# Performance work log

Hardware: AMD Instinct MI355X
Metric: run time of the kernel (lower is better)

Reference implementation:

```python
import jax, jax.numpy as jnp
import numpy as np

DT_RANK, D_STATE, D_INNER, D_MODEL, MAMBA_SQE = 32, 16, 128, 64, 12
CHUNKS = (4, 4, 4)


def conv2d(x, w, stride=1, pad=1, groups=1, b=None):
    out = jax.lax.conv_general_dilated(x, w, (stride, stride), [(pad, pad), (pad, pad)],
                                       dimension_numbers=('NCHW', 'OIHW', 'NCHW'),
                                       feature_group_count=groups)
    return out if b is None else out + b[None, :, None, None]


def batchnorm(x, g, b, eps=1e-5):
    # training-mode BN: biased batch stats over (N, H, W)
    m = x.mean((0, 2, 3), keepdims=True)
    v = ((x - m) ** 2).mean((0, 2, 3), keepdims=True)
    return (x - m) * jax.lax.rsqrt(v + eps) * g[None, :, None, None] + b[None, :, None, None]


def layernorm(x, g, b, eps=1e-5):
    m = x.mean(-1, keepdims=True)
    v = ((x - m) ** 2).mean(-1, keepdims=True)
    return (x - m) * jax.lax.rsqrt(v + eps) * g + b


def mamba_chunk(x, state, in_w, conv_w, conv_b, xproj_w, dt_w, dt_b, A_log, D, out_w):
    # x: (B, L, d_model); state: (B, d_inner, d_state). Selective scan seeded with carried ssm_state.
    xz = jnp.einsum('bld,ed->ble', x, in_w)            # (B, L, 2*d_inner)
    xi, z = jnp.split(xz, 2, axis=-1)
    xi = jax.nn.silu(xi * conv_w + conv_b)             # depthwise conv1d with d_conv=1
    xdb = jnp.einsum('bld,ed->ble', xi, xproj_w)       # (B, L, dt_rank + 2*d_state)
    dt = xdb[..., :DT_RANK]
    Bm = xdb[..., DT_RANK:DT_RANK + D_STATE]
    Cm = xdb[..., DT_RANK + D_STATE:]
    dt = jax.nn.softplus(jnp.einsum('blr,dr->bld', dt, dt_w) + dt_b)  # (B, L, d_inner)
    A = -jnp.exp(A_log)                                # (d_inner, d_state)

    def step(st, inp):
        dt_t, x_t, B_t, C_t = inp
        dA = jnp.exp(dt_t[:, :, None] * A)             # (B, d_inner, d_state)
        st = st * dA + (dt_t * x_t)[:, :, None] * B_t[:, None, :]
        y = jnp.einsum('bdn,bn->bd', st, C_t) + D * x_t
        return st, y

    state, ys = jax.lax.scan(step, state, (dt.transpose(1, 0, 2), xi.transpose(1, 0, 2),
                                           Bm.transpose(1, 0, 2), Cm.transpose(1, 0, 2)))
    y = ys.transpose(1, 0, 2) * jax.nn.silu(z)
    return jnp.einsum('bld,ed->ble', y, out_w), state


def _forward(features, high_feature, fid0, fid1, bn_in_g, bn_in_b, down_w, down_bn_g, down_bn_b,
             emb_w, emb_b, ln1_g, ln1_b, m_in_w, m_conv_w, m_conv_b, m_xproj_w, m_dt_w, m_dt_b,
             m_A_log, m_D, m_out_w, ln2_g, ln2_b, dec_w, dec_b, up0_w, up0_bn_g, up0_bn_b,
             up1_w, up1_bn_g, up1_bn_b, fus0_w, fus0_b, fus0_bn_g, fus0_bn_b,
             fus1_w, fus1_b, fus1_bn_g, fus1_bn_b, outf_w, outf_b, expanded_ratio, out_sqe_num):
    f = features + jnp.tile(high_feature, (1, expanded_ratio, 1, 1))
    f = jnp.concatenate([high_feature, f], axis=1)          # index != 'd3_0'
    f = batchnorm(f, bn_in_g, bn_in_b)
    # downsample_size = 1
    f = jax.nn.silu(batchnorm(conv2d(f, down_w, stride=2, groups=MAMBA_SQE), down_bn_g, down_bn_b))
    f = conv2d(f, emb_w, groups=MAMBA_SQE, b=emb_b)          # (b, 12*64, h, w)
    b_, c_, h_, w_ = f.shape
    tok = f.transpose(0, 2, 3, 1).reshape(b_ * h_ * w_, MAMBA_SQE, D_MODEL)  # (b h w) s d
    mfi = tok[:, -out_sqe_num:]
    tok = layernorm(tok, ln1_g, ln1_b)
    state = jnp.zeros((b_ * h_ * w_, D_INNER, D_STATE), dtype=tok.dtype)
    outs, off, record = [], 0, False
    for i, L in enumerate(CHUNKS):
        if off == MAMBA_SQE - out_sqe_num:
            record = True
        o, state = mamba_chunk(tok[:, off:off + L], state, m_in_w[i], m_conv_w[i], m_conv_b[i],
                               m_xproj_w[i], m_dt_w[i], m_dt_b[i], m_A_log[i], m_D[i], m_out_w[i])
        if record:
            outs.append(o)
        off += L
    y = layernorm(mfi + jnp.concatenate(outs, axis=1), ln2_g, ln2_b)  # (B, out_sqe_num, d)
    y = y.reshape(b_, h_, w_, out_sqe_num * D_MODEL).transpose(0, 3, 1, 2)
    y = conv2d(y, dec_w, groups=4, b=dec_b)                  # (b, 128, h, w)
    finals = []
    for mid, fid, (uw, ug, ub), (fw, fb, fg, fbb) in zip(
            (y[:, :64], y[:, 64:]), (fid0, fid1),
            ((up0_w, up0_bn_g, up0_bn_b), (up1_w, up1_bn_g, up1_bn_b)),
            ((fus0_w, fus0_b, fus0_bn_g, fus0_bn_b), (fus1_w, fus1_b, fus1_bn_g, fus1_bn_b))):
        m = jnp.repeat(jnp.repeat(mid, 2, axis=2), 2, axis=3)  # nearest x2 (2**downsample_size)
        m = jax.nn.silu(batchnorm(conv2d(m, uw, pad=0), ug, ub))
        m = jnp.concatenate([m, fid], axis=1)
        m = jax.nn.silu(batchnorm(conv2d(m, fw, b=fb), fg, fbb))
        finals.append(m)
    out = conv2d(jnp.concatenate(finals, axis=1), outf_w, pad=0, b=outf_b)
    return jax.nn.silu(out)


def setup_inputs():
    ks = iter(jax.random.split(jax.random.key(0), 64))
    r = lambda shape, s=0.05: s * jax.random.normal(next(ks), shape, dtype=jnp.float32)
    inp = {}
    inp['features'] = jax.random.normal(next(ks), (10, 192, 64, 64), dtype=jnp.float32)
    inp['high_feature'] = jax.random.normal(next(ks), (10, 48, 64, 64), dtype=jnp.float32)
    inp['fid0'] = jax.random.normal(next(ks), (10, 64, 64, 64), dtype=jnp.float32)
    inp['fid1'] = jax.random.normal(next(ks), (10, 64, 64, 64), dtype=jnp.float32)
    inp['bn_in_g'] = 1.0 + r((240,), 0.01); inp['bn_in_b'] = r((240,), 0.01)
    inp['down_w'] = r((384, 20, 3, 3))
    inp['down_bn_g'] = 1.0 + r((384,), 0.01); inp['down_bn_b'] = r((384,), 0.01)
    inp['emb_w'] = r((768, 32, 3, 3)); inp['emb_b'] = r((768,))
    inp['ln1_g'] = 1.0 + r((64,), 0.01); inp['ln1_b'] = r((64,), 0.01)
    inp['m_in_w'] = r((3, 256, 64))
    inp['m_conv_w'] = 1.0 + r((3, 128), 0.01); inp['m_conv_b'] = r((3, 128), 0.01)
    inp['m_xproj_w'] = r((3, 64, 128)); inp['m_dt_w'] = r((3, 128, 32))
    inp['m_dt_b'] = jnp.full((3, 128), -2.0) + r((3, 128), 0.01)
    inp['m_A_log'] = jnp.tile(jnp.log(jnp.arange(1.0, 17.0, dtype=jnp.float32)), (3, 128, 1))
    inp['m_D'] = 1.0 + r((3, 128), 0.01); inp['m_out_w'] = r((3, 64, 128))
    inp['ln2_g'] = 1.0 + r((64,), 0.01); inp['ln2_b'] = r((64,), 0.01)
    inp['dec_w'] = r((128, 64, 3, 3)); inp['dec_b'] = r((128,))
    inp['up0_w'] = r((64, 64, 1, 1)); inp['up0_bn_g'] = 1.0 + r((64,), 0.01); inp['up0_bn_b'] = r((64,), 0.01)
    inp['up1_w'] = r((64, 64, 1, 1)); inp['up1_bn_g'] = 1.0 + r((64,), 0.01); inp['up1_bn_b'] = r((64,), 0.01)
    inp['fus0_w'] = r((64, 128, 3, 3)); inp['fus0_b'] = r((64,))
    inp['fus0_bn_g'] = 1.0 + r((64,), 0.01); inp['fus0_bn_b'] = r((64,), 0.01)
    inp['fus1_w'] = r((64, 128, 3, 3)); inp['fus1_b'] = r((64,))
    inp['fus1_bn_g'] = 1.0 + r((64,), 0.01); inp['fus1_bn_b'] = r((64,), 0.01)
    inp['outf_w'] = r((64, 128, 1, 1)); inp['outf_b'] = r((64,))
    inp['expanded_ratio'] = 4
    inp['out_sqe_num'] = 4
    return inp


def reference(features, high_feature, fid0, fid1, bn_in_g, bn_in_b, down_w, down_bn_g, down_bn_b,
              emb_w, emb_b, ln1_g, ln1_b, m_in_w, m_conv_w, m_conv_b, m_xproj_w, m_dt_w, m_dt_b,
              m_A_log, m_D, m_out_w, ln2_g, ln2_b, dec_w, dec_b, up0_w, up0_bn_g, up0_bn_b,
              up1_w, up1_bn_g, up1_bn_b, fus0_w, fus0_b, fus0_bn_g, fus0_bn_b,
              fus1_w, fus1_b, fus1_bn_g, fus1_bn_b, outf_w, outf_b, expanded_ratio, out_sqe_num):
    return _forward(features, high_feature, fid0, fid1, bn_in_g, bn_in_b, down_w, down_bn_g, down_bn_b,
                    emb_w, emb_b, ln1_g, ln1_b, m_in_w, m_conv_w, m_conv_b, m_xproj_w, m_dt_w, m_dt_b,
                    m_A_log, m_D, m_out_w, ln2_g, ln2_b, dec_w, dec_b, up0_w, up0_bn_g, up0_bn_b,
                    up1_w, up1_bn_g, up1_bn_b, fus0_w, fus0_b, fus0_bn_g, fus0_bn_b,
                    fus1_w, fus1_b, fus1_bn_g, fus1_bn_b, outf_w, outf_b, expanded_ratio, out_sqe_num)
```

## Files before the change

### kernel.cpp

```cpp
#include <hip/hip_runtime.h>
#include <math.h>

static __device__ __forceinline__ float silu_f(float x){
    return x * __builtin_amdgcn_rcpf(1.f + __expf(-x));
}
static __device__ __forceinline__ float softplus_f(float x){
    return (x > 20.f) ? x : __logf(1.f + __expf(x));
}

#define OFF_INT    8192u
#define OFF_WDTT   57344u
#define OFF_BCT    106496u
#define OFF_OUTT   118784u
#define OFF_A2     126976u
#define OFF_DECIN  5251072u
#define OFF_DOWN   9838592u
#define OFF_DECOUT 9838592u
#define OFF_UC0    11149312u
#define OFF_UC1    11804672u
#define OFF_TOK    13770752u
#define OFF_FUS0   13770752u
#define OFF_FUS1   16392192u

__global__ __launch_bounds__(256) void k_bn_in(const float* __restrict__ feat,
// ... 134 lines not shown
        float x6 = tp[34], x7 = tp[35], x8 = tp[36];
        const float* wpi = wb + i*9;
        #pragma unroll
        for (int oo = 0; oo < 8; ++oo){
            const float* wp = wpi + (size_t)oo*180;
            acc[oo] = fmaf(x0, wp[0], acc[oo]);
            acc[oo] = fmaf(x1, wp[1], acc[oo]);
            acc[oo] = fmaf(x2, wp[2], acc[oo]);
            acc[oo] = fmaf(x3, wp[3], acc[oo]);
            acc[oo] = fmaf(x4, wp[4], acc[oo]);
            acc[oo] = fmaf(x5, wp[5], acc[oo]);
            acc[oo] = fmaf(x6, wp[6], acc[oo]);
            acc[oo] = fmaf(x7, wp[7], acc[oo]);
            acc[oo] = fmaf(x8, wp[8], acc[oo]);
        }
    }

    int oh = oh0 + sh, ow = ow0 + sw;
    float* op = out + ((size_t)b*384 + g*32 + og*8)*1024 + (oh << 5) + ow;
    #pragma unroll
    for (int oo = 0; oo < 8; ++oo) op[(size_t)oo*1024] = acc[oo];
}

__global__ __launch_bounds__(256) void k_emb(const float* __restrict__ down_act,
                                             const float* __restrict__ w,
                                             const float* __restrict__ bias,
                                             float* __restrict__ tok){
    __shared__ float ts[3200];
    int bt = blockIdx.x;
    int b  = bt / 192;
    int rem = bt - b*192;
    int g  = rem >> 4;
    int tIdx = rem & 15;
    int oh0 = (tIdx >> 2) << 3, ow0 = (tIdx & 3) << 3;
    int tid = threadIdx.x;

    for (int j = tid; j < 3200; j += 256){
        int i = j / 100, p = j - i*100;
        int ph = p / 10, pw = p - ph*10;
        int gh = oh0 + ph - 1, gw = ow0 + pw - 1;
        float v = 0.f;
        if (gh >= 0 && gh < 32 && gw >= 0 && gw < 32)
            v = down_act[((size_t)b*384 + g*32 + i)*1024 + (gh << 5) + gw];
        ts[j] = v;
    }
    __syncthreads();

    int og = __builtin_amdgcn_readfirstlane(tid >> 6);
    int sp = tid & 63, sh = sp >> 3, sw = sp & 7;
    const float* wb = w + ((size_t)g*64 + og*16)*288;
    const float* bb = bias + g*64 + og*16;

    float acc[16];
    #pragma unroll
    for (int oo = 0; oo < 16; ++oo) acc[oo] = bb[oo];

    const float* tbase = ts + sh*10 + sw;
    #pragma unroll 2
    for (int i = 0; i < 32; ++i){
        const float* tp = tbase + i*100;
        float x0 = tp[0],  x1 = tp[1],  x2 = tp[2];
        float x3 = tp[10], x4 = tp[11], x5 = tp[12];
        float x6 = tp[20], x7 = tp[21], x8 = tp[22];
        const float* wpi = wb + i*9;
        #pragma unroll
        for (int oo = 0; oo < 16; ++oo){
// ... 42 lines not shown
        int c = j >> 14, rem = j & 16383;
        int d = rem >> 7, ch = rem & 127;
        const float* dwr = dt_w + (size_t)(c*128 + ch)*32;
        const float* xw  = xproj_w + (size_t)c*8192 + d;
        float acc = 0.f;
        #pragma unroll
        for (int r = 0; r < 32; ++r) acc = fmaf(dwr[r], xw[(size_t)r*128], acc);
        WdtT[j] = acc;
    } else if (idx < 110592){
        int j = idx - 98304;
        int c = j >> 12, rem = j & 4095;
        int d = rem >> 5, e = rem & 31;
        bcT[j] = xproj_w[((size_t)(c*64 + 32 + e))*128 + d];
    } else if (idx < 118784){
        int j = idx - 110592;
        int ch = j >> 6, e = j & 63;
        outT[j] = out_w[((size_t)(128 + e))*128 + ch];
    } else {
        int j = idx - 118784;
        A2[j] = -expf(A_log[j]);
    }
}

__global__ __launch_bounds__(128) void k_mamba8(const float* __restrict__ tok,
                                                const float* __restrict__ inT,
                                                const float* __restrict__ conv_w,
                                                const float* __restrict__ conv_b,
                                                const float* __restrict__ WdtT,
                                                const float* __restrict__ bcT,
                                                const float* __restrict__ dt_b,
                                                const float* __restrict__ A2,
                                                const float* __restrict__ Dp,
                                                const float* __restrict__ outT,
                                                const float* __restrict__ ln1_g,
                                                const float* __restrict__ ln1_b,
                                                const float* __restrict__ ln2_g,
                                                const float* __restrict__ ln2_b,
                                                float* __restrict__ dec_in){
    int token = blockIdx.x;
    int tid   = threadIdx.x;
    int lane  = tid & 63, wv = tid >> 6;
    int ch    = tid;

    __shared__ float xs[12][64];
    __shared__ float raw[4][64];
    __shared__ float xi[12][128];
    __shared__ float bcs[4][32];
    __shared__ float yz[4][128];

    const float* trow = tok + (size_t)token*768;
    for (int r = wv; r < 12; r += 2){
        float v = trow[r*64 + lane];
        if (r >= 8) raw[r-8][lane] = v;
        float m  = wsum64(v) * (1.f/64.f);
        float dv = v - m;
        float var = wsum64(dv*dv) * (1.f/64.f);
        xs[r][lane] = dv*rsqrtf(var + 1e-5f)*ln1_g[lane] + ln1_b[lane];
    }
    __syncthreads();

    for (int c = 0; c < 3; ++c){
        const float* wp = inT + (size_t)c*16384 + ch;
        float a0=0.f, a1=0.f, a2=0.f, a3=0.f;
        int s0 = c*4;
        #pragma unroll 2
        for (int d4 = 0; d4 < 16; ++d4){
            float w0 = wp[(d4*4+0)*256], w1 = wp[(d4*4+1)*256];
            float w2 = wp[(d4*4+2)*256], w3 = wp[(d4*4+3)*256];
            float4 x0 = *(const float4*)&xs[s0+0][d4*4];
            float4 x1 = *(const float4*)&xs[s0+1][d4*4];
            float4 x2 = *(const float4*)&xs[s0+2][d4*4];
            float4 x3 = *(const float4*)&xs[s0+3][d4*4];
            a0 = fmaf(x0.x,w0, fmaf(x0.y,w1, fmaf(x0.z,w2, fmaf(x0.w,w3, a0))));
            a1 = fmaf(x1.x,w0, fmaf(x1.y,w1, fmaf(x1.z,w2, fmaf(x1.w,w3, a1))));
            a2 = fmaf(x2.x,w0, fmaf(x2.y,w1, fmaf(x2.z,w2, fmaf(x2.w,w3, a2))));
            a3 = fmaf(x3.x,w0, fmaf(x3.y,w1, fmaf(x3.z,w2, fmaf(x3.w,w3, a3))));
        }
        float cw = conv_w[c*128 + ch], cb = conv_b[c*128 + ch];
        xi[s0+0][ch] = silu_f(fmaf(a0, cw, cb));
        xi[s0+1][ch] = silu_f(fmaf(a1, cw, cb));
        xi[s0+2][ch] = silu_f(fmaf(a2, cw, cb));
        xi[s0+3][ch] = silu_f(fmaf(a3, cw, cb));
    }
    float zr0=0.f, zr1=0.f, zr2=0.f, zr3=0.f;
    {
        const float* wp = inT + (size_t)2*16384 + 128 + ch;
        #pragma unroll 2
        for (int d4 = 0; d4 < 16; ++d4){
            float w0 = wp[(d4*4+0)*256], w1 = wp[(d4*4+1)*256];
            float w2 = wp[(d4*4+2)*256], w3 = wp[(d4*4+3)*256];
            float4 x0 = *(const float4*)&xs[8][d4*4];
            float4 x1 = *(const float4*)&xs[9][d4*4];
            float4 x2 = *(const float4*)&xs[10][d4*4];
            float4 x3 = *(const float4*)&xs[11][d4*4];
            zr0 = fmaf(x0.x,w0, fmaf(x0.y,w1, fmaf(x0.z,w2, fmaf(x0.w,w3, zr0))));
            zr1 = fmaf(x1.x,w0, fmaf(x1.y,w1, fmaf(x1.z,w2, fmaf(x1.w,w3, zr1))));
            zr2 = fmaf(x2.x,w0, fmaf(x2.y,w1, fmaf(x2.z,w2, fmaf(x2.w,w3, zr2))));
            zr3 = fmaf(x3.x,w0, fmaf(x3.y,w1, fmaf(x3.z,w2, fmaf(x3.w,w3, zr3))));
        }
        zr0 = silu_f(zr0); zr1 = silu_f(zr1); zr2 = silu_f(zr2); zr3 = silu_f(zr3);
    }
    __syncthreads();

    int sidx = tid >> 5, be = tid & 31;
    float st[16];
    #pragma unroll
    for (int n = 0; n < 16; ++n) st[n] = 0.f;

    for (int c = 0; c < 3; ++c){
        int s0 = c*4;
        float dts0, dts1, dts2, dts3;
        {
            const float* wp = WdtT + (size_t)c*16384 + ch;
            float a0=0.f, a1=0.f, a2=0.f, a3=0.f;
            #pragma unroll 2
            for (int d4 = 0; d4 < 32; ++d4){
                float w0 = wp[(d4*4+0)*128], w1 = wp[(d4*4+1)*128];
                float w2 = wp[(d4*4+2)*128], w3 = wp[(d4*4+3)*128];
                float4 x0 = *(const float4*)&xi[s0+0][d4*4];
                float4 x1 = *(const float4*)&xi[s0+1][d4*4];
                float4 x2 = *(const float4*)&xi[s0+2][d4*4];
                float4 x3 = *(const float4*)&xi[s0+3][d4*4];
                a0 = fmaf(x0.x,w0, fmaf(x0.y,w1, fmaf(x0.z,w2, fmaf(x0.w,w3, a0))));
                a1 = fmaf(x1.x,w0, fmaf(x1.y,w1, fmaf(x1.z,w2, fmaf(x1.w,w3, a1))));
                a2 = fmaf(x2.x,w0, fmaf(x2.y,w1, fmaf(x2.z,w2, fmaf(x2.w,w3, a2))));
                a3 = fmaf(x3.x,w0, fmaf(x3.y,w1, fmaf(x3.z,w2, fmaf(x3.w,w3, a3))));
            }
            float db = dt_b[c*128 + ch];
            dts0 = softplus_f(a0 + db);
            dts1 = softplus_f(a1 + db);
            dts2 = softplus_f(a2 + db);
            dts3 = softplus_f(a3 + db);
        }
        float bcacc = 0.f;
        {
            const float* wp = bcT + (size_t)c*4096 + be;
            #pragma unroll 2
            for (int d4 = 0; d4 < 32; ++d4){
                float w0 = wp[(d4*4+0)*32], w1 = wp[(d4*4+1)*32];
                float w2 = wp[(d4*4+2)*32], w3 = wp[(d4*4+3)*32];
                float4 x = *(const float4*)&xi[s0+sidx][d4*4];
                bcacc = fmaf(x.x,w0, fmaf(x.y,w1, fmaf(x.z,w2, fmaf(x.w,w3, bcacc))));
            }
        }
        __syncthreads();
        bcs[sidx][be] = bcacc;
        __syncthreads();

        float A_[16];
        {
            const float4* ap = (const float4*)(A2 + ((size_t)c*128 + ch)*16);
            float4 a0v = ap[0], a1v = ap[1], a2v = ap[2], a3v = ap[3];
            A_[0]=a0v.x; A_[1]=a0v.y; A_[2]=a0v.z; A_[3]=a0v.w;
            A_[4]=a1v.x; A_[5]=a1v.y; A_[6]=a1v.z; A_[7]=a1v.w;
            A_[8]=a2v.x; A_[9]=a2v.y; A_[10]=a2v.z; A_[11]=a2v.w;
            A_[12]=a3v.x; A_[13]=a3v.y; A_[14]=a3v.z; A_[15]=a3v.w;
        }
        float Dch = Dp[c*128 + ch];

        #pragma unroll
        for (int t = 0; t < 4; ++t){
            float dtc = (t==0)?dts0:((t==1)?dts1:((t==2)?dts2:dts3));
            float xiv = xi[s0+t][ch];
            float dx  = dtc * xiv;
            float4 b0 = *(const float4*)&bcs[t][0];
            float4 b1 = *(const float4*)&bcs[t][4];
            float4 b2 = *(const float4*)&bcs[t][8];
            float4 b3 = *(const float4*)&bcs[t][12];
            if (c < 2){
                st[0] = fmaf(st[0],  __expf(dtc*A_[0]),  dx*b0.x);
                st[1] = fmaf(st[1],  __expf(dtc*A_[1]),  dx*b0.y);
                st[2] = fmaf(st[2],  __expf(dtc*A_[2]),  dx*b0.z);
                st[3] = fmaf(st[3],  __expf(dtc*A_[3]),  dx*b0.w);
                st[4] = fmaf(st[4],  __expf(dtc*A_[4]),  dx*b1.x);
                st[5] = fmaf(st[5],  __expf(dtc*A_[5]),  dx*b1.y);
                st[6] = fmaf(st[6],  __expf(dtc*A_[6]),  dx*b1.z);
                st[7] = fmaf(st[7],  __expf(dtc*A_[7]),  dx*b1.w);
                st[8] = fmaf(st[8],  __expf(dtc*A_[8]),  dx*b2.x);
                st[9] = fmaf(st[9],  __expf(dtc*A_[9]),  dx*b2.y);
                st[10]= fmaf(st[10], __expf(dtc*A_[10]), dx*b2.z);
                st[11]= fmaf(st[11], __expf(dtc*A_[11]), dx*b2.w);
                st[12]= fmaf(st[12], __expf(dtc*A_[12]), dx*b3.x);
                st[13]= fmaf(st[13], __expf(dtc*A_[13]), dx*b3.y);
                st[14]= fmaf(st[14], __expf(dtc*A_[14]), dx*b3.z);
                st[15]= fmaf(st[15], __expf(dtc*A_[15]), dx*b3.w);
            } else {
                float4 c0 = *(const float4*)&bcs[t][16];
                float4 c1 = *(const float4*)&bcs[t][20];
                float4 c2 = *(const float4*)&bcs[t][24];
                float4 c3 = *(const float4*)&bcs[t][28];
                float y = 0.f;
                st[0] = fmaf(st[0],  __expf(dtc*A_[0]),  dx*b0.x); y = fmaf(st[0],  c0.x, y);
                st[1] = fmaf(st[1],  __expf(dtc*A_[1]),  dx*b0.y); y = fmaf(st[1],  c0.y, y);
                st[2] = fmaf(st[2],  __expf(dtc*A_[2]),  dx*b0.z); y = fmaf(st[2],  c0.z, y);
                st[3] = fmaf(st[3],  __expf(dtc*A_[3]),  dx*b0.w); y = fmaf(st[3],  c0.w, y);
                st[4] = fmaf(st[4],  __expf(dtc*A_[4]),  dx*b1.x); y = fmaf(st[4],  c1.x, y);
                st[5] = fmaf(st[5],  __expf(dtc*A_[5]),  dx*b1.y); y = fmaf(st[5],  c1.y, y);
                st[6] = fmaf(st[6],  __expf(dtc*A_[6]),  dx*b1.z); y = fmaf(st[6],  c1.z, y);
                st[7] = fmaf(st[7],  __expf(dtc*A_[7]),  dx*b1.w); y = fmaf(st[7],  c1.w, y);
                st[8] = fmaf(st[8],  __expf(dtc*A_[8]),  dx*b2.x); y = fmaf(st[8],  c2.x, y);
                st[9] = fmaf(st[9],  __expf(dtc*A_[9]),  dx*b2.y); y = fmaf(st[9],  c2.y, y);
                st[10]= fmaf(st[10], __expf(dtc*A_[10]), dx*b2.z); y = fmaf(st[10], c2.z, y);
                st[11]= fmaf(st[11], __expf(dtc*A_[11]), dx*b2.w); y = fmaf(st[11], c2.w, y);
                st[12]= fmaf(st[12], __expf(dtc*A_[12]), dx*b3.x); y = fmaf(st[12], c3.x, y);
                st[13]= fmaf(st[13], __expf(dtc*A_[13]), dx*b3.y); y = fmaf(st[13], c3.y, y);
                st[14]= fmaf(st[14], __expf(dtc*A_[14]), dx*b3.z); y = fmaf(st[14], c3.z, y);
                st[15]= fmaf(st[15], __expf(dtc*A_[15]), dx*b3.w); y = fmaf(st[15], c3.w, y);
                y = fmaf(Dch, xiv, y);
                float zr = (t==0)?zr0:((t==1)?zr1:((t==2)?zr2:zr3));
                yz[t][ch] = y * zr;
            }
        }
    }
    __syncthreads();

    int b = token >> 10, hw = token & 1023;
    int e = tid & 63, l2 = tid >> 6;
    #pragma unroll
    for (int p = 0; p < 2; ++p){
        int l = l2*2 + p;
        float acc = 0.f;
        const float* wp = outT + e;
        #pragma unroll 2
        for (int k4 = 0; k4 < 32; ++k4){
            float w0 = wp[(k4*4+0)*64], w1 = wp[(k4*4+1)*64];
            float w2 = wp[(k4*4+2)*64], w3 = wp[(k4*4+3)*64];
            float4 y = *(const float4*)&yz[l][k4*4];
            acc = fmaf(y.x,w0, fmaf(y.y,w1, fmaf(y.z,w2, fmaf(y.w,w3, acc))));
        }
        float v = raw[l][e] + acc;
        float m  = wsum64(v) * (1.f/64.f);
        float dv = v - m;
        float var = wsum64(dv*dv) * (1.f/64.f);
        float r = dv*rsqrtf(var + 1e-5f)*ln2_g[e] + ln2_b[e];
        dec_in[(size_t)b*262144 + (size_t)(l*64 + e)*1024 + hw] = r;
    }
}

__global__ __launch_bounds__(256) void k_dec(const float* __restrict__ dec_in,
                                             const float* __restrict__ w,
                                             const float* __restrict__ bias,
                                             float* __restrict__ out){
    __shared__ float ts[6400];
    int bt = blockIdx.x;
    int b  = bt >> 6;
    int rem = bt & 63;
    int g  = rem >> 4;
    int tIdx = rem & 15;
    int oh0 = (tIdx >> 2) << 3, ow0 = (tIdx & 3) << 3;
    int tid = threadIdx.x;

    for (int j = tid; j < 6400; j += 256){
        int i = j / 100, p = j - i*100;
        int ph = p / 10, pw = p - ph*10;
        int gh = oh0 + ph - 1, gw = ow0 + pw - 1;
        float v = 0.f;
        if (gh >= 0 && gh < 32 && gw >= 0 && gw < 32)
            v = dec_in[((size_t)b*256 + g*64 + i)*1024 + (gh << 5) + gw];
// ... 41 lines not shown

__global__ __launch_bounds__(256) void k_up(const float* __restrict__ dec_out,
                                            const float* __restrict__ w0,
                                            const float* __restrict__ w1,
                                            float* __restrict__ uc0,
                                            float* __restrict__ uc1){
    int idx = blockIdx.x*256 + threadIdx.x;
    int r = idx >= 655360;
    int j = idx - r*655360;
    int b   = j / 65536;
    int rem = j - b*65536;
    int o   = rem >> 10;
    int hw  = rem & 1023;
    __shared__ float w_s[64];
    if (threadIdx.x < 64) w_s[threadIdx.x] = (r ? w1 : w0)[o*64 + threadIdx.x];
    __syncthreads();
    const float* in = dec_out + (size_t)b*131072 + (size_t)(r*64)*1024 + hw;
    float acc = 0.f;
    #pragma unroll 8
    for (int i = 0; i < 64; ++i) acc = fmaf(in[(size_t)i*1024], w_s[i], acc);
    (r ? uc1 : uc0)[j] = acc;
}

__global__ __launch_bounds__(256) void k_fus(const float* __restrict__ uc_act,
                                             const float* __restrict__ fid,
                                             const float* __restrict__ w,
                                             const float* __restrict__ bias,
                                             float* __restrict__ out){
    __shared__ float ts[12800];
    int bt = blockIdx.x;
    int b  = bt >> 6, tIdx = bt & 63;
    int oh0 = (tIdx >> 3) << 3, ow0 = (tIdx & 7) << 3;
    int tid = threadIdx.x;

    for (int j = tid; j < 12800; j += 256){
        int i = j / 100, p = j - i*100;
        int ph = p / 10, pw = p - ph*10;
        int gh = oh0 + ph - 1, gw = ow0 + pw - 1;
        float v = 0.f;
        if (gh >= 0 && gh < 64 && gw >= 0 && gw < 64){
            if (i < 64) v = uc_act[(((size_t)b*64 + i) << 10) + ((gh >> 1) << 5) + (gw >> 1)];
            else        v = fid[(((size_t)b*64 + i - 64) << 12) + (gh << 6) + gw];
        }
        ts[j] = v;
    }
    __syncthreads();

    int og = __builtin_amdgcn_readfirstlane(tid >> 6);
    int sp = tid & 63, sh = sp >> 3, sw = sp & 7;
    const float* wb = w + (size_t)og * 18432;
    const float* bb = bias + og * 16;

    float acc[16];
    #pragma unroll
    for (int oo = 0; oo < 16; ++oo) acc[oo] = bb[oo];

    const float* tbase = ts + sh*10 + sw;
    #pragma unroll 2
    for (int i = 0; i < 128; ++i){
        const float* tp = tbase + i*100;
        float x0 = tp[0],  x1 = tp[1],  x2 = tp[2];
        float x3 = tp[10], x4 = tp[11], x5 = tp[12];
        float x6 = tp[20], x7 = tp[21], x8 = tp[22];
        const float* wpi = wb + i*9;
        #pragma unroll
// ... 95 lines not shown
    float* st_u1_sc  = ws + 1664; float* st_u1_sh  = ws + 1728;
    float* st_f0_sc  = ws + 1792; float* st_f0_sh  = ws + 1856;
    float* st_f1_sc  = ws + 1920; float* st_f1_sh  = ws + 1984;

    float* inT    = ws + OFF_INT;
    float* WdtT   = ws + OFF_WDTT;
    float* bcT    = ws + OFF_BCT;
    float* outT   = ws + OFF_OUTT;
    float* A2     = ws + OFF_A2;
    float* dec_in = ws + OFF_DECIN;
    float* down   = ws + OFF_DOWN;
    float* dec_out= ws + OFF_DECOUT;
    float* uc0    = ws + OFF_UC0;
    float* uc1    = ws + OFF_UC1;
    float* tok    = ws + OFF_TOK;
    float* fus0   = ws + OFF_FUS0;
    float* fus1   = ws + OFF_FUS1;

    k_prep<<<488, 256, 0, stream>>>(m_in_w, m_dt_w, m_xproj_w, m_out_w, m_A_log,
                                    inT, WdtT, bcT, outT, A2);
    k_bn_in<<<240, 256, 0, stream>>>(features, high, bn_in_g, bn_in_b, st_in_sc, st_in_sh);
    k_down<<<1920, 256, 0, stream>>>(features, high, down_w, st_in_sc, st_in_sh, down);
    k_bn_stats<<<384, 256, 0, stream>>>(down, down_bn_g, down_bn_b, st_dn_sc, st_dn_sh, 384, 10, 10);
    k_affine_silu<<<15360, 256, 0, stream>>>(down, st_dn_sc, st_dn_sh, 384, 10, 3932160);
    k_emb<<<1920, 256, 0, stream>>>(down, emb_w, emb_b, tok);
    k_mamba8<<<10240, 128, 0, stream>>>(tok, inT, m_conv_w, m_conv_b, WdtT, bcT,
                                        m_dt_b, A2, m_D, outT,
                                        ln1_g, ln1_b, ln2_g, ln2_b, dec_in);
    k_dec<<<640, 256, 0, stream>>>(dec_in, dec_w, dec_b, dec_out);
    k_up<<<5120, 256, 0, stream>>>(dec_out, up0_w, up1_w, uc0, uc1);
    k_bn_stats<<<64, 256, 0, stream>>>(uc0, up0_bn_g, up0_bn_b, st_u0_sc, st_u0_sh, 64, 10, 10);
    k_bn_stats<<<64, 256, 0, stream>>>(uc1, up1_bn_g, up1_bn_b, st_u1_sc, st_u1_sh, 64, 10, 10);
    k_affine_silu<<<2560, 256, 0, stream>>>(uc0, st_u0_sc, st_u0_sh, 64, 10, 655360);
    k_affine_silu<<<2560, 256, 0, stream>>>(uc1, st_u1_sc, st_u1_sh, 64, 10, 655360);
    k_fus<<<640, 256, 0, stream>>>(uc0, fid0, fus0_w, fus0_b, fus0);
    k_fus<<<640, 256, 0, stream>>>(uc1, fid1, fus1_w, fus1_b, fus1);
    k_bn_stats<<<64, 256, 0, stream>>>(fus0, fus0_bn_g, fus0_bn_b, st_f0_sc, st_f0_sh, 64, 12, 10);
    k_bn_stats<<<64, 256, 0, stream>>>(fus1, fus1_bn_g, fus1_bn_b, st_f1_sc, st_f1_sh, 64, 12, 10);
    k_affine_silu<<<10240, 256, 0, stream>>>(fus0, st_f0_sc, st_f0_sh, 64, 12, 2621440);
    k_affine_silu<<<10240, 256, 0, stream>>>(fus1, st_f1_sc, st_f1_sh, 64, 12, 2621440);
    k_final<<<10240, 256, 0, stream>>>(fus0, fus1, outf_w, outf_b, out);
}
```

Before: 1.249 ms.

## Fuse BN-affine+SiLU into emb/fus loads and halve mamba block to one wave

The standalone BN affine+SiLU passes over the down-conv output and the two upsample outputs are removed. The affine and SiLU are now applied while k_emb and k_fus load their input tiles, which saves three elementwise kernels and their full read/write traffic. The mamba kernel is also reworked from 128 threads (one channel each) to 64 threads that each handle two channels. This doubles per-thread registers and serial work, but lets every weight load feed two channels and keeps the whole block in one wave. Because the halo tiles overlap, the fused kernels recompute SiLU on some elements, and the mamba change may lower occupancy.

```diff
diff --git a/kernel.cpp b/kernel.cpp
--- a/kernel.cpp
+++ b/kernel.cpp
@@ -180,7 +180,9 @@
     for (int oo = 0; oo < 8; ++oo) op[(size_t)oo*1024] = acc[oo];
 }
 
-__global__ __launch_bounds__(256) void k_emb(const float* __restrict__ down_act,
+__global__ __launch_bounds__(256) void k_emb(const float* __restrict__ down_raw,
+                                             const float* __restrict__ sc,
+                                             const float* __restrict__ sh_,
                                              const float* __restrict__ w,
                                              const float* __restrict__ bias,
                                              float* __restrict__ tok){
@@ -198,8 +200,11 @@
         int ph = p / 10, pw = p - ph*10;
         int gh = oh0 + ph - 1, gw = ow0 + pw - 1;
         float v = 0.f;
-        if (gh >= 0 && gh < 32 && gw >= 0 && gw < 32)
-            v = down_act[((size_t)b*384 + g*32 + i)*1024 + (gh << 5) + gw];
+        if (gh >= 0 && gh < 32 && gw >= 0 && gw < 32){
+            int c = g*32 + i;
+            float raw = down_raw[((size_t)b*384 + c)*1024 + (gh << 5) + gw];
+            v = silu_f(fmaf(raw, sc[c], sh_[c]));
+        }
         ts[j] = v;
     }
     __syncthreads();
@@ -288,25 +293,24 @@
     }
 }
 
-__global__ __launch_bounds__(128) void k_mamba8(const float* __restrict__ tok,
-                                                const float* __restrict__ inT,
-                                                const float* __restrict__ conv_w,
-                                                const float* __restrict__ conv_b,
-                                                const float* __restrict__ WdtT,
-                                                const float* __restrict__ bcT,
-                                                const float* __restrict__ dt_b,
-                                                const float* __restrict__ A2,
-                                                const float* __restrict__ Dp,
-                                                const float* __restrict__ outT,
-                                                const float* __restrict__ ln1_g,
-                                                const float* __restrict__ ln1_b,
-                                                const float* __restrict__ ln2_g,
-                                                const float* __restrict__ ln2_b,
-                                                float* __restrict__ dec_in){
+__global__ __launch_bounds__(64) void k_mamba9(const float* __restrict__ tok,
+                                               const float* __restrict__ inT,
+                                               const float* __restrict__ conv_w,
+                                               const float* __restrict__ conv_b,
+                                               const float* __restrict__ WdtT,
+                                               const float* __restrict__ bcT,
+                                               const float* __restrict__ dt_b,
+                                               const float* __restrict__ A2,
+                                               const float* __restrict__ Dp,
+                                               const float* __restrict__ outT,
+                                               const float* __restrict__ ln1_g,
+                                               const float* __restrict__ ln1_b,
+                                               const float* __restrict__ ln2_g,
+                                               const float* __restrict__ ln2_b,
+                                               float* __restrict__ dec_in){
     int token = blockIdx.x;
     int tid   = threadIdx.x;
-    int lane  = tid & 63, wv = tid >> 6;
-    int ch    = tid;
+    int ch0 = tid, ch1 = tid + 64;
 
     __shared__ float xs[12][64];
     __shared__ float raw[4][64];
@@ -315,24 +319,27 @@
     __shared__ float yz[4][128];
 
     const float* trow = tok + (size_t)token*768;
-    for (int r = wv; r < 12; r += 2){
-        float v = trow[r*64 + lane];
-        if (r >= 8) raw[r-8][lane] = v;
+    for (int r = 0; r < 12; ++r){
+        float v = trow[r*64 + tid];
+        if (r >= 8) raw[r-8][tid] = v;
         float m  = wsum64(v) * (1.f/64.f);
         float dv = v - m;
         float var = wsum64(dv*dv) * (1.f/64.f);
-        xs[r][lane] = dv*rsqrtf(var + 1e-5f)*ln1_g[lane] + ln1_b[lane];
+        xs[r][tid] = dv*rsqrtf(var + 1e-5f)*ln1_g[tid] + ln1_b[tid];
     }
     __syncthreads();
 
     for (int c = 0; c < 3; ++c){
-        const float* wp = inT + (size_t)c*16384 + ch;
+        const float* wp0 = inT + (size_t)c*16384 + ch0;
         float a0=0.f, a1=0.f, a2=0.f, a3=0.f;
+        float a4=0.f, a5=0.f, a6=0.f, a7=0.f;
         int s0 = c*4;
         #pragma unroll 2
         for (int d4 = 0; d4 < 16; ++d4){
-            float w0 = wp[(d4*4+0)*256], w1 = wp[(d4*4+1)*256];
-            float w2 = wp[(d4*4+2)*256], w3 = wp[(d4*4+3)*256];
+            float w0 = wp0[(d4*4+0)*256],    w1 = wp0[(d4*4+1)*256];
+            float w2 = wp0[(d4*4+2)*256],    w3 = wp0[(d4*4+3)*256];
+            float w4 = wp0[(d4*4+0)*256+64], w5 = wp0[(d4*4+1)*256+64];
+            float w6 = wp0[(d4*4+2)*256+64], w7 = wp0[(d4*4+3)*256+64];
             float4 x0 = *(const float4*)&xs[s0+0][d4*4];
             float4 x1 = *(const float4*)&xs[s0+1][d4*4];
             float4 x2 = *(const float4*)&xs[s0+2][d4*4];
@@ -341,48 +348,68 @@
             a1 = fmaf(x1.x,w0, fmaf(x1.y,w1, fmaf(x1.z,w2, fmaf(x1.w,w3, a1))));
             a2 = fmaf(x2.x,w0, fmaf(x2.y,w1, fmaf(x2.z,w2, fmaf(x2.w,w3, a2))));
             a3 = fmaf(x3.x,w0, fmaf(x3.y,w1, fmaf(x3.z,w2, fmaf(x3.w,w3, a3))));
-        }
-        float cw = conv_w[c*128 + ch], cb = conv_b[c*128 + ch];
-        xi[s0+0][ch] = silu_f(fmaf(a0, cw, cb));
-        xi[s0+1][ch] = silu_f(fmaf(a1, cw, cb));
-        xi[s0+2][ch] = silu_f(fmaf(a2, cw, cb));
-        xi[s0+3][ch] = silu_f(fmaf(a3, cw, cb));
-    }
-    float zr0=0.f, zr1=0.f, zr2=0.f, zr3=0.f;
+            a4 = fmaf(x0.x,w4, fmaf(x0.y,w5, fmaf(x0.z,w6, fmaf(x0.w,w7, a4))));
+            a5 = fmaf(x1.x,w4, fmaf(x1.y,w5, fmaf(x1.z,w6, fmaf(x1.w,w7, a5))));
+            a6 = fmaf(x2.x,w4, fmaf(x2.y,w5, fmaf(x2.z,w6, fmaf(x2.w,w7, a6))));
+            a7 = fmaf(x3.x,w4, fmaf(x3.y,w5, fmaf(x3.z,w6, fmaf(x3.w,w7, a7))));
+        }
+        float cw0 = conv_w[c*128 + ch0], cb0 = conv_b[c*128 + ch0];
+        float cw1 = conv_w[c*128 + ch1], cb1 = conv_b[c*128 + ch1];
+        xi[s0+0][ch0] = silu_f(fmaf(a0, cw0, cb0));
+        xi[s0+1][ch0] = silu_f(fmaf(a1, cw0, cb0));
+        xi[s0+2][ch0] = silu_f(fmaf(a2, cw0, cb0));
+        xi[s0+3][ch0] = silu_f(fmaf(a3, cw0, cb0));
+        xi[s0+0][ch1] = silu_f(fmaf(a4, cw1, cb1));
+        xi[s0+1][ch1] = silu_f(fmaf(a5, cw1, cb1));
+        xi[s0+2][ch1] = silu_f(fmaf(a6, cw1, cb1));
+        xi[s0+3][ch1] = silu_f(fmaf(a7, cw1, cb1));
+    }
+    float za0=0.f, za1=0.f, za2=0.f, za3=0.f;
+    float zb0=0.f, zb1=0.f, zb2=0.f, zb3=0.f;
     {
-        const float* wp = inT + (size_t)2*16384 + 128 + ch;
+        const float* wp0 = inT + (size_t)2*16384 + 128 + ch0;
         #pragma unroll 2
         for (int d4 = 0; d4 < 16; ++d4){
-            float w0 = wp[(d4*4+0)*256], w1 = wp[(d4*4+1)*256];
-            float w2 = wp[(d4*4+2)*256], w3 = wp[(d4*4+3)*256];
+            float w0 = wp0[(d4*4+0)*256],    w1 = wp0[(d4*4+1)*256];
+            float w2 = wp0[(d4*4+2)*256],    w3 = wp0[(d4*4+3)*256];
+            float w4 = wp0[(d4*4+0)*256+64], w5 = wp0[(d4*4+1)*256+64];
+            float w6 = wp0[(d4*4+2)*256+64], w7 = wp0[(d4*4+3)*256+64];
             float4 x0 = *(const float4*)&xs[8][d4*4];
             float4 x1 = *(const float4*)&xs[9][d4*4];
             float4 x2 = *(const float4*)&xs[10][d4*4];
             float4 x3 = *(const float4*)&xs[11][d4*4];
-            zr0 = fmaf(x0.x,w0, fmaf(x0.y,w1, fmaf(x0.z,w2, fmaf(x0.w,w3, zr0))));
-            zr1 = fmaf(x1.x,w0, fmaf(x1.y,w1, fmaf(x1.z,w2, fmaf(x1.w,w3, zr1))));
-            zr2 = fmaf(x2.x,w0, fmaf(x2.y,w1, fmaf(x2.z,w2, fmaf(x2.w,w3, zr2))));
-            zr3 = fmaf(x3.x,w0, fmaf(x3.y,w1, fmaf(x3.z,w2, fmaf(x3.w,w3, zr3))));
-        }
-        zr0 = silu_f(zr0); zr1 = silu_f(zr1); zr2 = silu_f(zr2); zr3 = silu_f(zr3);
+            za0 = fmaf(x0.x,w0, fmaf(x0.y,w1, fmaf(x0.z,w2, fmaf(x0.w,w3, za0))));
+            za1 = fmaf(x1.x,w0, fmaf(x1.y,w1, fmaf(x1.z,w2, fmaf(x1.w,w3, za1))));
+            za2 = fmaf(x2.x,w0, fmaf(x2.y,w1, fmaf(x2.z,w2, fmaf(x2.w,w3, za2))));
+            za3 = fmaf(x3.x,w0, fmaf(x3.y,w1, fmaf(x3.z,w2, fmaf(x3.w,w3, za3))));
+            zb0 = fmaf(x0.x,w4, fmaf(x0.y,w5, fmaf(x0.z,w6, fmaf(x0.w,w7, zb0))));
+            zb1 = fmaf(x1.x,w4, fmaf(x1.y,w5, fmaf(x1.z,w6, fmaf(x1.w,w7, zb1))));
+            zb2 = fmaf(x2.x,w4, fmaf(x2.y,w5, fmaf(x2.z,w6, fmaf(x2.w,w7, zb2))));
+            zb3 = fmaf(x3.x,w4, fmaf(x3.y,w5, fmaf(x3.z,w6, fmaf(x3.w,w7, zb3))));
+        }
+        za0 = silu_f(za0); za1 = silu_f(za1); za2 = silu_f(za2); za3 = silu_f(za3);
+        zb0 = silu_f(zb0); zb1 = silu_f(zb1); zb2 = silu_f(zb2); zb3 = silu_f(zb3);
     }
     __syncthreads();
 
     int sidx = tid >> 5, be = tid & 31;
-    float st[16];
-    #pragma unroll
-    for (int n = 0; n < 16; ++n) st[n] = 0.f;
+    float st0[16], st1[16];
+    #pragma unroll
+    for (int n = 0; n < 16; ++n){ st0[n] = 0.f; st1[n] = 0.f; }
 
     for (int c = 0; c < 3; ++c){
         int s0 = c*4;
-        float dts0, dts1, dts2, dts3;
+        float dA0, dA1, dA2, dA3, dB0, dB1, dB2, dB3;
         {
-            const float* wp = WdtT + (size_t)c*16384 + ch;
+            const float* wp0 = WdtT + (size_t)c*16384 + ch0;
             float a0=0.f, a1=0.f, a2=0.f, a3=0.f;
+            float a4=0.f, a5=0.f, a6=0.f, a7=0.f;
             #pragma unroll 2
             for (int d4 = 0; d4 < 32; ++d4){
-                float w0 = wp[(d4*4+0)*128], w1 = wp[(d4*4+1)*128];
-                float w2 = wp[(d4*4+2)*128], w3 = wp[(d4*4+3)*128];
+                float w0 = wp0[(d4*4+0)*128],    w1 = wp0[(d4*4+1)*128];
+                float w2 = wp0[(d4*4+2)*128],    w3 = wp0[(d4*4+3)*128];
+                float w4 = wp0[(d4*4+0)*128+64], w5 = wp0[(d4*4+1)*128+64];
+                float w6 = wp0[(d4*4+2)*128+64], w7 = wp0[(d4*4+3)*128+64];
                 float4 x0 = *(const float4*)&xi[s0+0][d4*4];
                 float4 x1 = *(const float4*)&xi[s0+1][d4*4];
                 float4 x2 = *(const float4*)&xi[s0+2][d4*4];
@@ -391,102 +418,147 @@
                 a1 = fmaf(x1.x,w0, fmaf(x1.y,w1, fmaf(x1.z,w2, fmaf(x1.w,w3, a1))));
                 a2 = fmaf(x2.x,w0, fmaf(x2.y,w1, fmaf(x2.z,w2, fmaf(x2.w,w3, a2))));
                 a3 = fmaf(x3.x,w0, fmaf(x3.y,w1, fmaf(x3.z,w2, fmaf(x3.w,w3, a3))));
+                a4 = fmaf(x0.x,w4, fmaf(x0.y,w5, fmaf(x0.z,w6, fmaf(x0.w,w7, a4))));
+                a5 = fmaf(x1.x,w4, fmaf(x1.y,w5, fmaf(x1.z,w6, fmaf(x1.w,w7, a5))));
+                a6 = fmaf(x2.x,w4, fmaf(x2.y,w5, fmaf(x2.z,w6, fmaf(x2.w,w7, a6))));
+                a7 = fmaf(x3.x,w4, fmaf(x3.y,w5, fmaf(x3.z,w6, fmaf(x3.w,w7, a7))));
             }
-            float db = dt_b[c*128 + ch];
-            dts0 = softplus_f(a0 + db);
-            dts1 = softplus_f(a1 + db);
-            dts2 = softplus_f(a2 + db);
-            dts3 = softplus_f(a3 + db);
-        }
-        float bcacc = 0.f;
+            float db0 = dt_b[c*128 + ch0], db1 = dt_b[c*128 + ch1];
+            dA0 = softplus_f(a0 + db0); dA1 = softplus_f(a1 + db0);
+            dA2 = softplus_f(a2 + db0); dA3 = softplus_f(a3 + db0);
+            dB0 = softplus_f(a4 + db1); dB1 = softplus_f(a5 + db1);
+            dB2 = softplus_f(a6 + db1); dB3 = softplus_f(a7 + db1);
+        }
+        float bc0 = 0.f, bc1 = 0.f;
         {
             const float* wp = bcT + (size_t)c*4096 + be;
             #pragma unroll 2
             for (int d4 = 0; d4 < 32; ++d4){
                 float w0 = wp[(d4*4+0)*32], w1 = wp[(d4*4+1)*32];
                 float w2 = wp[(d4*4+2)*32], w3 = wp[(d4*4+3)*32];
-                float4 x = *(const float4*)&xi[s0+sidx][d4*4];
-                bcacc = fmaf(x.x,w0, fmaf(x.y,w1, fmaf(x.z,w2, fmaf(x.w,w3, bcacc))));
+                float4 xA = *(const float4*)&xi[s0+sidx][d4*4];
+                float4 xB = *(const float4*)&xi[s0+sidx+2][d4*4];
+                bc0 = fmaf(xA.x,w0, fmaf(xA.y,w1, fmaf(xA.z,w2, fmaf(xA.w,w3, bc0))));
+                bc1 = fmaf(xB.x,w0, fmaf(xB.y,w1, fmaf(xB.z,w2, fmaf(xB.w,w3, bc1))));
             }
         }
         __syncthreads();
-        bcs[sidx][be] = bcacc;
+        bcs[sidx][be]   = bc0;
+        bcs[sidx+2][be] = bc1;
         __syncthreads();
 
-        float A_[16];
+        float A0_[16], A1_[16];
         {
-            const float4* ap = (const float4*)(A2 + ((size_t)c*128 + ch)*16);
-            float4 a0v = ap[0], a1v = ap[1], a2v = ap[2], a3v = ap[3];
-            A_[0]=a0v.x; A_[1]=a0v.y; A_[2]=a0v.z; A_[3]=a0v.w;
-            A_[4]=a1v.x; A_[5]=a1v.y; A_[6]=a1v.z; A_[7]=a1v.w;
-            A_[8]=a2v.x; A_[9]=a2v.y; A_[10]=a2v.z; A_[11]=a2v.w;
-            A_[12]=a3v.x; A_[13]=a3v.y; A_[14]=a3v.z; A_[15]=a3v.w;
-        }
-        float Dch = Dp[c*128 + ch];
+            const float4* ap0 = (const float4*)(A2 + ((size_t)c*128 + ch0)*16);
+            const float4* ap1 = (const float4*)(A2 + ((size_t)c*128 + ch1)*16);
+            #pragma unroll
+            for (int q = 0; q < 4; ++q){
+                float4 v0 = ap0[q], v1 = ap1[q];
+                A0_[q*4+0]=v0.x; A0_[q*4+1]=v0.y; A0_[q*4+2]=v0.z; A0_[q*4+3]=v0.w;
+                A1_[q*4+0]=v1.x; A1_[q*4+1]=v1.y; A1_[q*4+2]=v1.z; A1_[q*4+3]=v1.w;
+            }
+        }
+        float D0 = Dp[c*128 + ch0], D1 = Dp[c*128 + ch1];
 
         #pragma unroll
         for (int t = 0; t < 4; ++t){
-            float dtc = (t==0)?dts0:((t==1)?dts1:((t==2)?dts2:dts3));
-            float xiv = xi[s0+t][ch];
-            float dx  = dtc * xiv;
+            float dt0 = (t==0)?dA0:((t==1)?dA1:((t==2)?dA2:dA3));
+            float dt1 = (t==0)?dB0:((t==1)?dB1:((t==2)?dB2:dB3));
+            float xv0 = xi[s0+t][ch0];
+            float xv1 = xi[s0+t][ch1];
+            float dx0 = dt0 * xv0;
+            float dx1 = dt1 * xv1;
             float4 b0 = *(const float4*)&bcs[t][0];
             float4 b1 = *(const float4*)&bcs[t][4];
             float4 b2 = *(const float4*)&bcs[t][8];
             float4 b3 = *(const float4*)&bcs[t][12];
             if (c < 2){
-                st[0] = fmaf(st[0],  __expf(dtc*A_[0]),  dx*b0.x);
-                st[1] = fmaf(st[1],  __expf(dtc*A_[1]),  dx*b0.y);
-                st[2] = fmaf(st[2],  __expf(dtc*A_[2]),  dx*b0.z);
-                st[3] = fmaf(st[3],  __expf(dtc*A_[3]),  dx*b0.w);
-                st[4] = fmaf(st[4],  __expf(dtc*A_[4]),  dx*b1.x);
-                st[5] = fmaf(st[5],  __expf(dtc*A_[5]),  dx*b1.y);
-                st[6] = fmaf(st[6],  __expf(dtc*A_[6]),  dx*b1.z);
-                st[7] = fmaf(st[7],  __expf(dtc*A_[7]),  dx*b1.w);
-                st[8] = fmaf(st[8],  __expf(dtc*A_[8]),  dx*b2.x);
-                st[9] = fmaf(st[9],  __expf(dtc*A_[9]),  dx*b2.y);
-                st[10]= fmaf(st[10], __expf(dtc*A_[10]), dx*b2.z);
-                st[11]= fmaf(st[11], __expf(dtc*A_[11]), dx*b2.w);
-                st[12]= fmaf(st[12], __expf(dtc*A_[12]), dx*b3.x);
-                st[13]= fmaf(st[13], __expf(dtc*A_[13]), dx*b3.y);
-                st[14]= fmaf(st[14], __expf(dtc*A_[14]), dx*b3.z);
-                st[15]= fmaf(st[15], __expf(dtc*A_[15]), dx*b3.w);
+                st0[0] = fmaf(st0[0],  __expf(dt0*A0_[0]),  dx0*b0.x);
+                st0[1] = fmaf(st0[1],  __expf(dt0*A0_[1]),  dx0*b0.y);
+                st0[2] = fmaf(st0[2],  __expf(dt0*A0_[2]),  dx0*b0.z);
+                st0[3] = fmaf(st0[3],  __expf(dt0*A0_[3]),  dx0*b0.w);
+                st0[4] = fmaf(st0[4],  __expf(dt0*A0_[4]),  dx0*b1.x);
+                st0[5] = fmaf(st0[5],  __expf(dt0*A0_[5]),  dx0*b1.y);
+                st0[6] = fmaf(st0[6],  __expf(dt0*A0_[6]),  dx0*b1.z);
+                st0[7] = fmaf(st0[7],  __expf(dt0*A0_[7]),  dx0*b1.w);
+                st0[8] = fmaf(st0[8],  __expf(dt0*A0_[8]),  dx0*b2.x);
+                st0[9] = fmaf(st0[9],  __expf(dt0*A0_[9]),  dx0*b2.y);
+                st0[10]= fmaf(st0[10], __expf(dt0*A0_[10]), dx0*b2.z);
+                st0[11]= fmaf(st0[11], __expf(dt0*A0_[11]), dx0*b2.w);
+                st0[12]= fmaf(st0[12], __expf(dt0*A0_[12]), dx0*b3.x);
+                st0[13]= fmaf(st0[13], __expf(dt0*A0_[13]), dx0*b3.y);
+                st0[14]= fmaf(st0[14], __expf(dt0*A0_[14]), dx0*b3.z);
+                st0[15]= fmaf(st0[15], __expf(dt0*A0_[15]), dx0*b3.w);
+                st1[0] = fmaf(st1[0],  __expf(dt1*A1_[0]),  dx1*b0.x);
+                st1[1] = fmaf(st1[1],  __expf(dt1*A1_[1]),  dx1*b0.y);
+                st1[2] = fmaf(st1[2],  __expf(dt1*A1_[2]),  dx1*b0.z);
+                st1[3] = fmaf(st1[3],  __expf(dt1*A1_[3]),  dx1*b0.w);
+                st1[4] = fmaf(st1[4],  __expf(dt1*A1_[4]),  dx1*b1.x);
+                st1[5] = fmaf(st1[5],  __expf(dt1*A1_[5]),  dx1*b1.y);
+                st1[6] = fmaf(st1[6],  __expf(dt1*A1_[6]),  dx1*b1.z);
+                st1[7] = fmaf(st1[7],  __expf(dt1*A1_[7]),  dx1*b1.w);
+                st1[8] = fmaf(st1[8],  __expf(dt1*A1_[8]),  dx1*b2.x);
+                st1[9] = fmaf(st1[9],  __expf(dt1*A1_[9]),  dx1*b2.y);
+                st1[10]= fmaf(st1[10], __expf(dt1*A1_[10]), dx1*b2.z);
+                st1[11]= fmaf(st1[11], __expf(dt1*A1_[11]), dx1*b2.w);
+                st1[12]= fmaf(st1[12], __expf(dt1*A1_[12]), dx1*b3.x);
+                st1[13]= fmaf(st1[13], __expf(dt1*A1_[13]), dx1*b3.y);
+                st1[14]= fmaf(st1[14], __expf(dt1*A1_[14]), dx1*b3.z);
+                st1[15]= fmaf(st1[15], __expf(dt1*A1_[15]), dx1*b3.w);
             } else {
                 float4 c0 = *(const float4*)&bcs[t][16];
                 float4 c1 = *(const float4*)&bcs[t][20];
                 float4 c2 = *(const float4*)&bcs[t][24];
                 float4 c3 = *(const float4*)&bcs[t][28];
-                float y = 0.f;
-                st[0] = fmaf(st[0],  __expf(dtc*A_[0]),  dx*b0.x); y = fmaf(st[0],  c0.x, y);
-                st[1] = fmaf(st[1],  __expf(dtc*A_[1]),  dx*b0.y); y = fmaf(st[1],  c0.y, y);
-                st[2] = fmaf(st[2],  __expf(dtc*A_[2]),  dx*b0.z); y = fmaf(st[2],  c0.z, y);
-                st[3] = fmaf(st[3],  __expf(dtc*A_[3]),  dx*b0.w); y = fmaf(st[3],  c0.w, y);
-                st[4] = fmaf(st[4],  __expf(dtc*A_[4]),  dx*b1.x); y = fmaf(st[4],  c1.x, y);
-                st[5] = fmaf(st[5],  __expf(dtc*A_[5]),  dx*b1.y); y = fmaf(st[5],  c1.y, y);
-                st[6] = fmaf(st[6],  __expf(dtc*A_[6]),  dx*b1.z); y = fmaf(st[6],  c1.z, y);
-                st[7] = fmaf(st[7],  __expf(dtc*A_[7]),  dx*b1.w); y = fmaf(st[7],  c1.w, y);
-                st[8] = fmaf(st[8],  __expf(dtc*A_[8]),  dx*b2.x); y = fmaf(st[8],  c2.x, y);
-                st[9] = fmaf(st[9],  __expf(dtc*A_[9]),  dx*b2.y); y = fmaf(st[9],  c2.y, y);
-                st[10]= fmaf(st[10], __expf(dtc*A_[10]), dx*b2.z); y = fmaf(st[10], c2.z, y);
-                st[11]= fmaf(st[11], __expf(dtc*A_[11]), dx*b2.w); y = fmaf(st[11], c2.w, y);
-                st[12]= fmaf(st[12], __expf(dtc*A_[12]), dx*b3.x); y = fmaf(st[12], c3.x, y);
-                st[13]= fmaf(st[13], __expf(dtc*A_[13]), dx*b3.y); y = fmaf(st[13], c3.y, y);
-                st[14]= fmaf(st[14], __expf(dtc*A_[14]), dx*b3.z); y = fmaf(st[14], c3.z, y);
-                st[15]= fmaf(st[15], __expf(dtc*A_[15]), dx*b3.w); y = fmaf(st[15], c3.w, y);
-                y = fmaf(Dch, xiv, y);
-                float zr = (t==0)?zr0:((t==1)?zr1:((t==2)?zr2:zr3));
-                yz[t][ch] = y * zr;
+                float y0 = 0.f, y1 = 0.f;
+                st0[0] = fmaf(st0[0],  __expf(dt0*A0_[0]),  dx0*b0.x); y0 = fmaf(st0[0],  c0.x, y0);
+                st0[1] = fmaf(st0[1],  __expf(dt0*A0_[1]),  dx0*b0.y); y0 = fmaf(st0[1],  c0.y, y0);
+                st0[2] = fmaf(st0[2],  __expf(dt0*A0_[2]),  dx0*b0.z); y0 = fmaf(st0[2],  c0.z, y0);
+                st0[3] = fmaf(st0[3],  __expf(dt0*A0_[3]),  dx0*b0.w); y0 = fmaf(st0[3],  c0.w, y0);
+                st0[4] = fmaf(st0[4],  __expf(dt0*A0_[4]),  dx0*b1.x); y0 = fmaf(st0[4],  c1.x, y0);
+                st0[5] = fmaf(st0[5],  __expf(dt0*A0_[5]),  dx0*b1.y); y0 = fmaf(st0[5],  c1.y, y0);
+                st0[6] = fmaf(st0[6],  __expf(dt0*A0_[6]),  dx0*b1.z); y0 = fmaf(st0[6],  c1.z, y0);
+                st0[7] = fmaf(st0[7],  __expf(dt0*A0_[7]),  dx0*b1.w); y0 = fmaf(st0[7],  c1.w, y0);
+                st0[8] = fmaf(st0[8],  __expf(dt0*A0_[8]),  dx0*b2.x); y0 = fmaf(st0[8],  c2.x, y0);
+                st0[9] = fmaf(st0[9],  __expf(dt0*A0_[9]),  dx0*b2.y); y0 = fmaf(st0[9],  c2.y, y0);
+                st0[10]= fmaf(st0[10], __expf(dt0*A0_[10]), dx0*b2.z); y0 = fmaf(st0[10], c2.z, y0);
+                st0[11]= fmaf(st0[11], __expf(dt0*A0_[11]), dx0*b2.w); y0 = fmaf(st0[11], c2.w, y0);
+                st0[12]= fmaf(st0[12], __expf(dt0*A0_[12]), dx0*b3.x); y0 = fmaf(st0[12], c3.x, y0);
+                st0[13]= fmaf(st0[13], __expf(dt0*A0_[13]), dx0*b3.y); y0 = fmaf(st0[13], c3.y, y0);
+                st0[14]= fmaf(st0[14], __expf(dt0*A0_[14]), dx0*b3.z); y0 = fmaf(st0[14], c3.z, y0);
+                st0[15]= fmaf(st0[15], __expf(dt0*A0_[15]), dx0*b3.w); y0 = fmaf(st0[15], c3.w, y0);
+                st1[0] = fmaf(st1[0],  __expf(dt1*A1_[0]),  dx1*b0.x); y1 = fmaf(st1[0],  c0.x, y1);
+                st1[1] = fmaf(st1[1],  __expf(dt1*A1_[1]),  dx1*b0.y); y1 = fmaf(st1[1],  c0.y, y1);
+                st1[2] = fmaf(st1[2],  __expf(dt1*A1_[2]),  dx1*b0.z); y1 = fmaf(st1[2],  c0.z, y1);
+                st1[3] = fmaf(st1[3],  __expf(dt1*A1_[3]),  dx1*b0.w); y1 = fmaf(st1[3],  c0.w, y1);
+                st1[4] = fmaf(st1[4],  __expf(dt1*A1_[4]),  dx1*b1.x); y1 = fmaf(st1[4],  c1.x, y1);
+                st1[5] = fmaf(st1[5],  __expf(dt1*A1_[5]),  dx1*b1.y); y1 = fmaf(st1[5],  c1.y, y1);
+                st1[6] = fmaf(st1[6],  __expf(dt1*A1_[6]),  dx1*b1.z); y1 = fmaf(st1[6],  c1.z, y1);
+                st1[7] = fmaf(st1[7],  __expf(dt1*A1_[7]),  dx1*b1.w); y1 = fmaf(st1[7],  c1.w, y1);
+                st1[8] = fmaf(st1[8],  __expf(dt1*A1_[8]),  dx1*b2.x); y1 = fmaf(st1[8],  c2.x, y1);
+                st1[9] = fmaf(st1[9],  __expf(dt1*A1_[9]),  dx1*b2.y); y1 = fmaf(st1[9],  c2.y, y1);
+                st1[10]= fmaf(st1[10], __expf(dt1*A1_[10]), dx1*b2.z); y1 = fmaf(st1[10], c2.z, y1);
+                st1[11]= fmaf(st1[11], __expf(dt1*A1_[11]), dx1*b2.w); y1 = fmaf(st1[11], c2.w, y1);
+                st1[12]= fmaf(st1[12], __expf(dt1*A1_[12]), dx1*b3.x); y1 = fmaf(st1[12], c3.x, y1);
+                st1[13]= fmaf(st1[13], __expf(dt1*A1_[13]), dx1*b3.y); y1 = fmaf(st1[13], c3.y, y1);
+                st1[14]= fmaf(st1[14], __expf(dt1*A1_[14]), dx1*b3.z); y1 = fmaf(st1[14], c3.z, y1);
+                st1[15]= fmaf(st1[15], __expf(dt1*A1_[15]), dx1*b3.w); y1 = fmaf(st1[15], c3.w, y1);
+                y0 = fmaf(D0, xv0, y0);
+                y1 = fmaf(D1, xv1, y1);
+                float zr0v = (t==0)?za0:((t==1)?za1:((t==2)?za2:za3));
+                float zr1v = (t==0)?zb0:((t==1)?zb1:((t==2)?zb2:zb3));
+                yz[t][ch0] = y0 * zr0v;
+                yz[t][ch1] = y1 * zr1v;
             }
         }
     }
     __syncthreads();
 
     int b = token >> 10, hw = token & 1023;
-    int e = tid & 63, l2 = tid >> 6;
-    #pragma unroll
-    for (int p = 0; p < 2; ++p){
-        int l = l2*2 + p;
+    #pragma unroll
+    for (int l = 0; l < 4; ++l){
         float acc = 0.f;
-        const float* wp = outT + e;
+        const float* wp = outT + tid;
         #pragma unroll 2
         for (int k4 = 0; k4 < 32; ++k4){
             float w0 = wp[(k4*4+0)*64], w1 = wp[(k4*4+1)*64];
@@ -494,12 +566,12 @@
             float4 y = *(const float4*)&yz[l][k4*4];
             acc = fmaf(y.x,w0, fmaf(y.y,w1, fmaf(y.z,w2, fmaf(y.w,w3, acc))));
         }
-        float v = raw[l][e] + acc;
+        float v = raw[l][tid] + acc;
         float m  = wsum64(v) * (1.f/64.f);
         float dv = v - m;
         float var = wsum64(dv*dv) * (1.f/64.f);
-        float r = dv*rsqrtf(var + 1e-5f)*ln2_g[e] + ln2_b[e];
-        dec_in[(size_t)b*262144 + (size_t)(l*64 + e)*1024 + hw] = r;
+        float r = dv*rsqrtf(var + 1e-5f)*ln2_g[tid] + ln2_b[tid];
+        dec_in[(size_t)b*262144 + (size_t)(l*64 + tid)*1024 + hw] = r;
     }
 }
 
@@ -587,7 +659,9 @@
     (r ? uc1 : uc0)[j] = acc;
 }
 
-__global__ __launch_bounds__(256) void k_fus(const float* __restrict__ uc_act,
+__global__ __launch_bounds__(256) void k_fus(const float* __restrict__ uc_raw,
+                                             const float* __restrict__ uc_sc,
+                                             const float* __restrict__ uc_sh,
                                              const float* __restrict__ fid,
                                              const float* __restrict__ w,
                                              const float* __restrict__ bias,
@@ -604,8 +678,12 @@
         int gh = oh0 + ph - 1, gw = ow0 + pw - 1;
         float v = 0.f;
         if (gh >= 0 && gh < 64 && gw >= 0 && gw < 64){
-            if (i < 64) v = uc_act[(((size_t)b*64 + i) << 10) + ((gh >> 1) << 5) + (gw >> 1)];
-            else        v = fid[(((size_t)b*64 + i - 64) << 12) + (gh << 6) + gw];
+            if (i < 64){
+                float raw = uc_raw[(((size_t)b*64 + i) << 10) + ((gh >> 1) << 5) + (gw >> 1)];
+                v = silu_f(fmaf(raw, uc_sc[i], uc_sh[i]));
+            } else {
+                v = fid[(((size_t)b*64 + i - 64) << 12) + (gh << 6) + gw];
+            }
         }
         ts[j] = v;
     }
@@ -747,19 +825,16 @@
     k_bn_in<<<240, 256, 0, stream>>>(features, high, bn_in_g, bn_in_b, st_in_sc, st_in_sh);
     k_down<<<1920, 256, 0, stream>>>(features, high, down_w, st_in_sc, st_in_sh, down);
     k_bn_stats<<<384, 256, 0, stream>>>(down, down_bn_g, down_bn_b, st_dn_sc, st_dn_sh, 384, 10, 10);
-    k_affine_silu<<<15360, 256, 0, stream>>>(down, st_dn_sc, st_dn_sh, 384, 10, 3932160);
-    k_emb<<<1920, 256, 0, stream>>>(down, emb_w, emb_b, tok);
-    k_mamba8<<<10240, 128, 0, stream>>>(tok, inT, m_conv_w, m_conv_b, WdtT, bcT,
-                                        m_dt_b, A2, m_D, outT,
-                                        ln1_g, ln1_b, ln2_g, ln2_b, dec_in);
+    k_emb<<<1920, 256, 0, stream>>>(down, st_dn_sc, st_dn_sh, emb_w, emb_b, tok);
+    k_mamba9<<<10240, 64, 0, stream>>>(tok, inT, m_conv_w, m_conv_b, WdtT, bcT,
+                                       m_dt_b, A2, m_D, outT,
+                                       ln1_g, ln1_b, ln2_g, ln2_b, dec_in);
     k_dec<<<640, 256, 0, stream>>>(dec_in, dec_w, dec_b, dec_out);
     k_up<<<5120, 256, 0, stream>>>(dec_out, up0_w, up1_w, uc0, uc1);
     k_bn_stats<<<64, 256, 0, stream>>>(uc0, up0_bn_g, up0_bn_b, st_u0_sc, st_u0_sh, 64, 10, 10);
     k_bn_stats<<<64, 256, 0, stream>>>(uc1, up1_bn_g, up1_bn_b, st_u1_sc, st_u1_sh, 64, 10, 10);
-    k_affine_silu<<<2560, 256, 0, stream>>>(uc0, st_u0_sc, st_u0_sh, 64, 10, 655360);
-    k_affine_silu<<<2560, 256, 0, stream>>>(uc1, st_u1_sc, st_u1_sh, 64, 10, 655360);
-    k_fus<<<640, 256, 0, stream>>>(uc0, fid0, fus0_w, fus0_b, fus0);
-    k_fus<<<640, 256, 0, stream>>>(uc1, fid1, fus1_w, fus1_b, fus1);
+    k_fus<<<640, 256, 0, stream>>>(uc0, st_u0_sc, st_u0_sh, fid0, fus0_w, fus0_b, fus0);
+    k_fus<<<640, 256, 0, stream>>>(uc1, st_u1_sc, st_u1_sh, fid1, fus1_w, fus1_b, fus1);
     k_bn_stats<<<64, 256, 0, stream>>>(fus0, fus0_bn_g, fus0_bn_b, st_f0_sc, st_f0_sh, 64, 12, 10);
     k_bn_stats<<<64, 256, 0, stream>>>(fus1, fus1_bn_g, fus1_bn_b, st_f1_sc, st_f1_sh, 64, 12, 10);
     k_affine_silu<<<10240, 256, 0, stream>>>(fus0, st_f0_sc, st_f0_sh, 64, 12, 2621440);
```

New measurement: 1.236 ms. Within noise of the previous version (-1.0%).
